# Performance work log

Measured on AMD Instinct MI355X. Metric: run time of the kernel, lower is better.

Reference implementation:

```python
import jax, jax.numpy as jnp
import numpy as np

NLAT, NLON = 128, 256
C = 256
B = 2
THETA_CUTOFF = 5.0 * np.pi / NLAT


def _build_csr():
    # equiangular colatitudes (midpoint rule) and longitudes
    theta = (np.arange(NLAT) + 0.5) * np.pi / NLAT
    phi = 2.0 * np.pi * np.arange(NLON) / NLON
    cth, sth = np.cos(theta), np.sin(theta)
    cphi = np.cos(phi)
    cos_cut = np.cos(THETA_CUTOFF)
    rows, cols = [], []
    for ho in range(NLAT):
        # great-circle distance from output point (theta[ho], lon=0) to all inputs
        cosd = cth[ho] * cth[:, None] + sth[ho] * sth[:, None] * cphi[None, :]
        hi, wi = np.nonzero(cosd >= cos_cut)
        rows.append(np.full(hi.shape[0], ho, dtype=np.int64))
        cols.append(hi * NLON + wi)
    return np.concatenate(rows), np.concatenate(cols)


def setup_inputs() -> dict:
    key = jax.random.key(0)
    kq, kw1, kw2, kw3 = jax.random.split(key, 4)
    scale = float(np.sqrt(1.0 / C))
    query = jax.random.normal(kq, (B, C, NLAT, NLON), dtype=jnp.float32)
    q_w = scale * jax.random.normal(kw1, (C, C), dtype=jnp.float32)
    k_w = scale * jax.random.normal(kw2, (C, C), dtype=jnp.float32)
    v_w = scale * jax.random.normal(kw3, (C, C), dtype=jnp.float32)
    q_bias = jnp.zeros((C,), dtype=jnp.float32)
    k_bias = jnp.zeros((C,), dtype=jnp.float32)
    v_bias = jnp.zeros((C,), dtype=jnp.float32)
    # quadrature weights: 2*pi * wgl / nlon, wgl ~ sin(theta) normalized to sum to 2
    theta = (np.arange(NLAT) + 0.5) * np.pi / NLAT
    wgl = np.sin(theta)
    wgl = 2.0 * wgl / wgl.sum()
    quad_weights = jnp.asarray(2.0 * np.pi * wgl / NLON, dtype=jnp.float32)
    row_idx, col_idx = _build_csr()
    return {
        "query": query,
        "q_w": q_w, "k_w": k_w, "v_w": v_w,
        "q_bias": q_bias, "k_bias": k_bias, "v_bias": v_bias,
        "quad_weights": quad_weights,
        "psi_row_idx": jnp.asarray(row_idx, dtype=jnp.int32),
        "psi_col_idx": jnp.asarray(col_idx, dtype=jnp.int32),
    }


def reference(query, q_w, k_w, v_w, q_bias, k_bias, v_bias, quad_weights, psi_row_idx, psi_col_idx):
    Bq, Cin, H, W = query.shape
    Ck = q_w.shape[0]
    Cv = v_w.shape[0]
    scale = 1.0 / np.sqrt(Cin)  # module sets scale = sqrt(1/in_channels)
    # 1x1 conv2d projections == per-pixel channel GEMMs; query is pre-scaled
    q = jnp.einsum('kc,bchw->bkhw', q_w, query * scale) + q_bias[None, :, None, None]
    k = jnp.einsum('kc,bchw->bkhw', k_w, query) + k_bias[None, :, None, None]
    v = jnp.einsum('vc,bchw->bvhw', v_w, query) + v_bias[None, :, None, None]
    kf = k.reshape(Bq, Ck, H * W)
    vf = v.reshape(Bq, Cv, H * W)
    hi = psi_col_idx // W   # neighbor input latitude  [nnz]
    wi = psi_col_idx % W    # neighbor input longitude offset (at wo=0)
    rows = psi_row_idx      # output latitude per nnz (sorted)
    qw_nbr = quad_weights[hi]  # [nnz]

    def step(carry, wo):
        idx = hi * W + (wi + wo) % W                 # longitude-shifted neighbor gather
        kg = jnp.take(kf, idx, axis=2)               # [B,Ck,nnz]
        vg = jnp.take(vf, idx, axis=2)               # [B,Cv,nnz]
        qcol = jnp.take(q, wo, axis=3)               # [B,Ck,H]
        qr = qcol[:, :, rows]                        # [B,Ck,nnz]
        logits = jnp.einsum('bkn,bkn->nb', qr, kg)   # [nnz,B]
        m = jax.ops.segment_max(logits, rows, num_segments=H, indices_are_sorted=True)
        alpha = jnp.exp(logits - m[rows]) * qw_nbr[:, None]                     # quadrature-weighted softmax numerator
        denom = jax.ops.segment_sum(alpha, rows, num_segments=H, indices_are_sorted=True)  # [H,B]
        num = jax.ops.segment_sum(alpha[:, :, None] * jnp.transpose(vg, (2, 0, 1)), rows,
                                  num_segments=H, indices_are_sorted=True)      # [H,B,Cv]
        return carry, num / denom[:, :, None]

    _, cols = jax.lax.scan(step, None, jnp.arange(W))  # [W,H,B,Cv]
    return jnp.transpose(cols, (2, 3, 1, 0))           # [B,Cv,H,W]
```

## Files before the change

### kernel.cpp

```cpp
#include <hip/hip_runtime.h>
#include <hip/hip_bf16.h>
#include <cstdint>


#define NLAT 128
#define NLON 256
#define NCH  256
#define HWSZ (NLAT * NLON)
#define SEGN 11

typedef __attribute__((ext_vector_type(4))) float f32x4;
typedef __attribute__((ext_vector_type(8))) short s16x8;

__device__ __forceinline__ float bf2f(unsigned int hi_bits) {
    return __uint_as_float(hi_bits);
}
__device__ __forceinline__ unsigned short f2bf(float f) {
    unsigned int u = __float_as_uint(f);
    return (unsigned short)((u + 0x7fffu + ((u >> 16) & 1u)) >> 16);
}

__global__ void k_rowptr(const int* __restrict__ rows, int nnz, int* __restrict__ rp) {
    int ho = threadIdx.x;
    if (ho > NLAT) return;
    int lo = 0, hi = nnz;
    while (lo < hi) {
        int mid = (lo + hi) >> 1;
        if (rows[mid] < ho) lo = mid + 1; else hi = mid;
    }
    rp[ho] = lo;
}

__global__ __launch_bounds__(256) void k_qkv(
    const float* __restrict__ query,
    const float* __restrict__ qw, const float* __restrict__ kw, const float* __restrict__ vw,
    const float* __restrict__ qb, const float* __restrict__ kb, const float* __restrict__ vb,
    unsigned short* __restrict__ qB, unsigned short* __restrict__ kB, unsigned short* __restrict__ vT)
{
    __shared__ unsigned short As[256][40];
    __shared__ unsigned short Bs[64][264];

    const int n0  = blockIdx.x * 64;
    const int b   = n0 >> 15;
    const int hw0 = n0 & (HWSZ - 1);
    const float* qsrc = query + (size_t)b * NCH * HWSZ + hw0;

    const int tid  = threadIdx.x;
    const int lane = tid & 63;
    const int w    = tid >> 6;
    const int l15  = lane & 15;
    const int g    = lane >> 4;

    {
        const int n   = tid & 63;
        const int k0r = tid >> 6;
        #pragma unroll 8
        for (int it = 0; it < 64; ++it) {
            const int kk = k0r + it * 4;
            Bs[n][kk] = f2bf(qsrc[(size_t)kk * HWSZ + n]);
        }
    }

    const int la_m = tid >> 3;
    const int la_k = (tid & 7) * 4;

    for (int y = 0; y < 3; ++y) {
        const float* Wm; const float* bias; float scale;
        if (y == 0)      { Wm = qw; bias = qb; scale = 0.0625f; }
        else if (y == 1) { Wm = kw; bias = kb; scale = 1.0f; }
        else             { Wm = vw; bias = vb; scale = 1.0f; }

        f32x4 acc[4][4] = {};

        for (int ks = 0; ks < 8; ++ks) {
            const int k0 = ks * 32;
            __syncthreads();
            #pragma unroll
            for (int r = 0; r < 8; ++r) {
                const int m = la_m + r * 32;
                const float4 v = *(const float4*)(Wm + (size_t)m * NCH + k0 + la_k);
                ushort4 st;
                st.x = f2bf(v.x * scale); st.y = f2bf(v.y * scale);
                st.z = f2bf(v.z * scale); st.w = f2bf(v.w * scale);
                *(ushort4*)&As[m][la_k] = st;
            }
            __syncthreads();

            s16x8 af[4], bfr[4];
            #pragma unroll
            for (int i = 0; i < 4; ++i)
                af[i] = *(const s16x8*)&As[w * 64 + i * 16 + l15][g * 8];
            #pragma unroll
            for (int j = 0; j < 4; ++j)
                bfr[j] = *(const s16x8*)&Bs[j * 16 + l15][k0 + g * 8];
            #pragma unroll
            for (int i = 0; i < 4; ++i)
                #pragma unroll
                for (int j = 0; j < 4; ++j)
                    acc[i][j] = __builtin_amdgcn_mfma_f32_16x16x32_bf16(af[i], bfr[j], acc[i][j], 0, 0, 0);
        }

        const int mrow = (g) * 4;
        if (y == 2) {
            const int h = hw0 >> 8;
            const int wbase = hw0 & 255;
            #pragma unroll
            for (int i = 0; i < 4; ++i) {
                const int m0 = w * 64 + i * 16 + mrow;
                const float4 bv = *(const float4*)(bias + m0);
                #pragma unroll
                for (int j = 0; j < 4; ++j) {
                    const int wc = wbase + j * 16 + l15;
                    const size_t rowb = ((size_t)((b * 128 + h) * 256 + m0)) << 8;
                    vT[rowb + wc]       = f2bf(acc[i][j][0] + bv.x);
                    vT[rowb + 256 + wc] = f2bf(acc[i][j][1] + bv.y);
                    vT[rowb + 512 + wc] = f2bf(acc[i][j][2] + bv.z);
                    vT[rowb + 768 + wc] = f2bf(acc[i][j][3] + bv.w);
                }
            }
        } else {
            unsigned short* outp = (y == 0) ? qB : kB;
            #pragma unroll
            for (int i = 0; i < 4; ++i) {
                const int m0 = w * 64 + i * 16 + mrow;
                const float4 bv = *(const float4*)(bias + m0);
                #pragma unroll
                for (int j = 0; j < 4; ++j) {
                    const int n = j * 16 + l15;
                    ushort4 st;
                    st.x = f2bf(acc[i][j][0] + bv.x);
                    st.y = f2bf(acc[i][j][1] + bv.y);
                    st.z = f2bf(acc[i][j][2] + bv.z);
                    st.w = f2bf(acc[i][j][3] + bv.w);
                    *(ushort4*)(outp + (((size_t)(b * HWSZ + hw0 + n)) << 8) + m0) = st;
                }
            }
        }
    }
}

__global__ __launch_bounds__(256, 2) void k_attn(
    const unsigned short* __restrict__ qB,
    const unsigned short* __restrict__ kB,
    const unsigned short* __restrict__ vT,
    const int* __restrict__ psi_col,
    const float* __restrict__ qwt,
    const int* __restrict__ rp,
    float* __restrict__ out)
{
    __shared__ unsigned int   segmask[SEGN][8];
    __shared__ int seg_dlo[SEGN], seg_ext[SEGN];
    __shared__ unsigned short als[4][16][40];
    __shared__ float Osm[128][68];

    const int bid  = blockIdx.x;
    const int orig = (bid & 7) * 128 + (bid >> 3);
    const int b    = orig >> 9;
    const int ho   = (orig >> 2) & 127;
    const int wo0  = (orig & 3) * 64;

    const int tid  = threadIdx.x;
    const int lane = tid & 63;
    const int wv   = tid >> 6;
    const int l15  = lane & 15;
    const int g    = lane >> 4;

    for (int i = tid; i < SEGN * 8; i += 256) ((unsigned*)segmask)[i] = 0u;
    __syncthreads();
    const int r0 = rp[ho], r1 = rp[ho + 1];
    for (int n = r0 + tid; n < r1; n += 256) {
        const int col = psi_col[n];
        const int s = (col >> 8) - ho + 5;
        if ((unsigned)s < SEGN) atomicOr(&segmask[s][(col & 255) >> 5], 1u << (col & 31));
    }
    __syncthreads();
    if (tid < SEGN) {
        const int hi = ho - 5 + tid;
        int dlo = 0, ext = 0;
        if (hi >= 0 && hi < 128) {
            unsigned mw[8]; int pc = 0;
            for (int w = 0; w < 8; ++w) { mw[w] = segmask[tid][w]; pc += __popc(mw[w]); }
            if (pc >= 256) { dlo = 0; ext = 256; }
            else if (pc > 0) {
                int t = 0; bool run = true;
                for (int w = 0; w < 8; ++w) {
                    if (!run) break;
                    if (mw[w] == 0xffffffffu) t += 32;
                    else { t += __ffs(~mw[w]) - 1; run = false; }
                }
                int z = 0; run = true;
                for (int w = 7; w >= 0; --w) {
                    if (!run) break;
                    if (mw[w] == 0xffffffffu) z += 32;
                    else { z += __clz(~mw[w]); run = false; }
                }
                if (pc == t + z && t + z <= 256) { dlo = -z; ext = pc; }
                else { dlo = 0; ext = 256; }
            }
        }
        seg_dlo[tid] = dlo; seg_ext[tid] = ext;
    }
    __syncthreads();

    const int ws0 = wo0 + wv * 16;
    const size_t qpt = ((size_t)(b * HWSZ + ho * 256 + ws0 + l15)) << 8;
    s16x8 af[8];
    #pragma unroll
    for (int ck = 0; ck < 8; ++ck) af[ck] = *(const s16x8*)(qB + qpt + ck * 32 + g * 8);

    f32x4 O[16] = {};
    float M[4] = {-1e38f, -1e38f, -1e38f, -1e38f};
    float L[4] = {0.f, 0.f, 0.f, 0.f};

    const size_t kbb = ((size_t)(b * HWSZ)) << 8;
    const unsigned short* vbb = vT + (((size_t)(b * 128)) << 8) * 256;

    for (int s = 0; s < SEGN; ++s) {
        const int ext = seg_ext[s];
        if (ext == 0) continue;
        const int dlo = seg_dlo[s];
        const int hi  = ho - 5 + s;
        const float qw = qwt[hi];
        const unsigned mk0 = __builtin_amdgcn_readfirstlane(segmask[s][0]);
        const unsigned mk1 = __builtin_amdgcn_readfirstlane(segmask[s][1]);
        const unsigned mk2 = __builtin_amdgcn_readfirstlane(segmask[s][2]);
        const unsigned mk3 = __builtin_amdgcn_readfirstlane(segmask[s][3]);
        const unsigned mk4 = __builtin_amdgcn_readfirstlane(segmask[s][4]);
        const unsigned mk5 = __builtin_amdgcn_readfirstlane(segmask[s][5]);
        const unsigned mk6 = __builtin_amdgcn_readfirstlane(segmask[s][6]);
        const unsigned mk7 = __builtin_amdgcn_readfirstlane(segmask[s][7]);

        const int dlo8 = dlo & ~7;
        const int pad  = dlo - dlo8;
        int jtot = 15 + pad + ext; if (jtot > 256) jtot = 256;
        const int wbase = (ws0 + dlo8) & 255;
        const unsigned short* kptr = kB + kbb + (((size_t)(hi * 256)) << 8);
        const unsigned short* vptr = vbb + (((size_t)(hi * 256)) << 8);

        for (int j0 = 0; j0 < jtot; j0 += 32) {
            f32x4 S[2];
            __builtin_amdgcn_s_setprio(1);
            #pragma unroll
            for (int jt = 0; jt < 2; ++jt) {
                const int wil = (wbase + j0 + jt * 16 + l15) & 255;
                const unsigned short* kp = kptr + (((size_t)wil) << 8) + g * 8;
                f32x4 a = {};
                #pragma unroll
                for (int ck = 0; ck < 8; ++ck) {
                    const s16x8 bf = *(const s16x8*)(kp + ck * 32);
                    a = __builtin_amdgcn_mfma_f32_16x16x32_bf16(af[ck], bf, a, 0, 0, 0);
                }
                S[jt] = a;
            }
            __builtin_amdgcn_s_setprio(0);

            #pragma unroll
            for (int jt = 0; jt < 2; ++jt) {
                const int tbase = dlo8 + j0 + jt * 16 + l15 - 4 * g;
                #pragma unroll
                for (int r = 0; r < 4; ++r) {
                    const int wi = (tbase - r) & 255;
                    const unsigned sel = (wi & 0x80)
                        ? ((wi & 0x40) ? ((wi & 0x20) ? mk7 : mk6) : ((wi & 0x20) ? mk5 : mk4))
                        : ((wi & 0x40) ? ((wi & 0x20) ? mk3 : mk2) : ((wi & 0x20) ? mk1 : mk0));
                    if (!((sel >> (wi & 31)) & 1u)) S[jt][r] = -3e38f;
                }
            }

            float rmax[4];
            #pragma unroll
            for (int r = 0; r < 4; ++r) {
                float v = fmaxf(S[0][r], S[1][r]);
                v = fmaxf(v, __shfl_xor(v, 1));
                v = fmaxf(v, __shfl_xor(v, 2));
                v = fmaxf(v, __shfl_xor(v, 4));
                v = fmaxf(v, __shfl_xor(v, 8));
                rmax[r] = v;
            }
            int need = 0;
            #pragma unroll
            for (int r = 0; r < 4; ++r) need |= (rmax[r] > M[r] + 8.0f) ? 1 : 0;
            if (__any(need)) {
                #pragma unroll
                for (int r = 0; r < 4; ++r) {
                    const float Mn = fmaxf(M[r], rmax[r]);
                    const float f = __expf(M[r] - Mn);
                    M[r] = Mn; L[r] *= f;
                    #pragma unroll
                    for (int ct = 0; ct < 16; ++ct) O[ct][r] *= f;
                }
            }

            #pragma unroll
            for (int jt = 0; jt < 2; ++jt) {
                #pragma unroll
                for (int r = 0; r < 4; ++r) {
                    const float a = qw * __expf(S[jt][r] - M[r]);
                    const unsigned short ab = f2bf(a);
                    L[r] += bf2f(((unsigned)ab) << 16);
                    als[wv][4 * g + r][jt * 16 + l15] = ab;
                }
            }
            const s16x8 afr = *(const s16x8*)&als[wv][l15][g * 8];

            const int wj = (wbase + j0 + g * 8) & 255;
            __builtin_amdgcn_s_setprio(1);
            #pragma unroll
            for (int ct = 0; ct < 16; ++ct) {
                const s16x8 vb8 = *(const s16x8*)(vptr + (((size_t)(ct * 16 + l15)) << 8) + wj);
                O[ct] = __builtin_amdgcn_mfma_f32_16x16x32_bf16(afr, vb8, O[ct], 0, 0, 0);
            }
            __builtin_amdgcn_s_setprio(0);
        }
    }

    float rL[4];
    #pragma unroll
    for (int r = 0; r < 4; ++r) {
        float v = L[r];
        v += __shfl_xor(v, 1);
        v += __shfl_xor(v, 2);
        v += __shfl_xor(v, 4);
        v += __shfl_xor(v, 8);
        rL[r] = 1.0f / v;
    }
    __syncthreads();
    #pragma unroll
    for (int p = 0; p < 2; ++p) {
        #pragma unroll
        for (int ci = 0; ci < 8; ++ci) {
            const int ct = p * 8 + ci;
            #pragma unroll
            for (int r = 0; r < 4; ++r)
                Osm[ci * 16 + l15][wv * 16 + 4 * g + r] = O[ct][r] * rL[r];
        }
        __syncthreads();
        const int m4 = (tid & 15) * 4;
        #pragma unroll
        for (int ci = 0; ci < 8; ++ci) {
            const int crow = ci * 16 + (tid >> 4);
            const int c = p * 128 + crow;
            const f32x4 o = *(const f32x4*)&Osm[crow][m4];
            *(f32x4*)(out + (((size_t)((b * NCH + c) * NLAT + ho)) << 8) + wo0 + m4) = o;
        }
        __syncthreads();
    }
}

extern "C" void kernel_launch(void* const* d_in, const int* in_sizes, int n_in,
                              void* d_out, int out_size, void* d_ws, size_t ws_size,
                              hipStream_t stream) {
    const float* query = (const float*)d_in[0];
    const float* q_w   = (const float*)d_in[1];
    const float* k_w   = (const float*)d_in[2];
    const float* v_w   = (const float*)d_in[3];
    const float* q_b   = (const float*)d_in[4];
    const float* k_b   = (const float*)d_in[5];
    const float* v_b   = (const float*)d_in[6];
    const float* qwt   = (const float*)d_in[7];
    const int* psi_row = (const int*)d_in[8];
    const int* psi_col = (const int*)d_in[9];
    const int nnz      = in_sizes[8];

    char* ws = (char*)d_ws;
    unsigned short* qB = (unsigned short*)(ws);
    unsigned short* kB = (unsigned short*)(ws + 33554432);
    unsigned short* vT = (unsigned short*)(ws + 67108864);
    int* rp            = (int*)(ws + 100663296);

    k_rowptr<<<dim3(1), dim3(256), 0, stream>>>(psi_row, nnz, rp);
    k_qkv<<<dim3(1024), dim3(256), 0, stream>>>(query, q_w, k_w, v_w, q_b, k_b, v_b, qB, kB, vT);
    k_attn<<<dim3(1024), dim3(256), 0, stream>>>(qB, kB, vT, psi_col, qwt, rp, (float*)d_out);
}
```

Baseline: 643.0 us.

## Split QKV projection into prep transpose and grid-tiled GEMM, simplify attention epilogue

A new prep kernel transposes the input to channel-last bf16 (staged in the output buffer), converts the weights to bf16, and computes the row pointers. The QKV GEMM then runs on a 3D grid reading bf16 operands straight from global memory, with a small shared-memory transpose for the V output. The attention kernel now maps latitude rows to XCDs in a balanced way, stores output directly without the shared-memory staging, and raises occupancy to 4 blocks per CU. The changes target redundant per-block weight conversion and epilogue synchronisation, at the cost of an extra full pass over the input and uncoalesced output stores.

```diff
diff --git a/kernel.cpp b/kernel.cpp
--- a/kernel.cpp
+++ b/kernel.cpp
@@ -20,126 +20,134 @@
     return (unsigned short)((u + 0x7fffu + ((u >> 16) & 1u)) >> 16);
 }
 
-__global__ void k_rowptr(const int* __restrict__ rows, int nnz, int* __restrict__ rp) {
-    int ho = threadIdx.x;
-    if (ho > NLAT) return;
-    int lo = 0, hi = nnz;
-    while (lo < hi) {
-        int mid = (lo + hi) >> 1;
-        if (rows[mid] < ho) lo = mid + 1; else hi = mid;
-    }
-    rp[ho] = lo;
-}
-
-__global__ __launch_bounds__(256) void k_qkv(
+__global__ __launch_bounds__(256) void k_prep(
     const float* __restrict__ query,
     const float* __restrict__ qw, const float* __restrict__ kw, const float* __restrict__ vw,
+    const int* __restrict__ rows, int nnz,
+    unsigned short* __restrict__ qT, unsigned short* __restrict__ Wbf, int* __restrict__ rp)
+{
+    const int bid = blockIdx.x;
+    const int tid = threadIdx.x;
+    if (bid < 4096) {
+        __shared__ unsigned short T[64][66];
+        const int b   = bid >> 11;
+        const int ct  = (bid >> 9) & 3;
+        const int hw0 = (bid & 511) * 64;
+        const float* src = query + (size_t)b * NCH * HWSZ + (size_t)(ct * 64) * HWSZ + hw0;
+        const int hw_l = tid & 63;
+        const int csub = tid >> 6;
+        #pragma unroll
+        for (int r = 0; r < 16; ++r) {
+            const int c_l = r * 4 + csub;
+            T[c_l][hw_l] = f2bf(src[(size_t)c_l * HWSZ + hw_l]);
+        }
+        __syncthreads();
+        const int c_l2 = tid & 63;
+        const int hsub = tid >> 6;
+        #pragma unroll
+        for (int r = 0; r < 16; ++r) {
+            const int hw_l2 = r * 4 + hsub;
+            qT[((size_t)(b * HWSZ + hw0 + hw_l2) << 8) + ct * 64 + c_l2] = T[c_l2][hw_l2];
+        }
+    } else if (bid < 4099) {
+        const int y = bid - 4096;
+        const float* src = (y == 0) ? qw : (y == 1) ? kw : vw;
+        const float scale = (y == 0) ? 0.0625f : 1.0f;
+        unsigned short* dst = Wbf + y * 65536;
+        for (int i = tid; i < 65536; i += 256) dst[i] = f2bf(src[i] * scale);
+    } else {
+        const int ho = tid;
+        if (ho > NLAT) return;
+        int lo = 0, hi = nnz;
+        while (lo < hi) {
+            int mid = (lo + hi) >> 1;
+            if (rows[mid] < ho) lo = mid + 1; else hi = mid;
+        }
+        rp[ho] = lo;
+    }
+}
+
+__global__ __launch_bounds__(256, 2) void k_qkv(
+    const unsigned short* __restrict__ Wbf,
+    const unsigned short* __restrict__ qT,
     const float* __restrict__ qb, const float* __restrict__ kb, const float* __restrict__ vb,
     unsigned short* __restrict__ qB, unsigned short* __restrict__ kB, unsigned short* __restrict__ vT)
 {
-    __shared__ unsigned short As[256][40];
-    __shared__ unsigned short Bs[64][264];
-
-    const int n0  = blockIdx.x * 64;
-    const int b   = n0 >> 15;
-    const int hw0 = n0 & (HWSZ - 1);
-    const float* qsrc = query + (size_t)b * NCH * HWSZ + hw0;
-
+    __shared__ unsigned short Tv[4][16][18];
+    const int nt = blockIdx.x, mt = blockIdx.y, y = blockIdx.z;
     const int tid  = threadIdx.x;
     const int lane = tid & 63;
-    const int w    = tid >> 6;
+    const int wv   = tid >> 6;
     const int l15  = lane & 15;
     const int g    = lane >> 4;
-
-    {
-        const int n   = tid & 63;
-        const int k0r = tid >> 6;
-        #pragma unroll 8
-        for (int it = 0; it < 64; ++it) {
-            const int kk = k0r + it * 4;
-            Bs[n][kk] = f2bf(qsrc[(size_t)kk * HWSZ + n]);
-        }
-    }
-
-    const int la_m = tid >> 3;
-    const int la_k = (tid & 7) * 4;
-
-    for (int y = 0; y < 3; ++y) {
-        const float* Wm; const float* bias; float scale;
-        if (y == 0)      { Wm = qw; bias = qb; scale = 0.0625f; }
-        else if (y == 1) { Wm = kw; bias = kb; scale = 1.0f; }
-        else             { Wm = vw; bias = vb; scale = 1.0f; }
-
-        f32x4 acc[4][4] = {};
-
-        for (int ks = 0; ks < 8; ++ks) {
-            const int k0 = ks * 32;
-            __syncthreads();
-            #pragma unroll
-            for (int r = 0; r < 8; ++r) {
-                const int m = la_m + r * 32;
-                const float4 v = *(const float4*)(Wm + (size_t)m * NCH + k0 + la_k);
+    const int wm = wv >> 1, wn = wv & 1;
+
+    const int m0    = mt * 128 + wm * 64;
+    const int nbase = nt * 128 + wn * 64;
+    const unsigned short* Wy   = Wbf + y * 65536;
+    const unsigned short* qrow = qT + ((size_t)nbase << 8);
+    const float* bias = (y == 0) ? qb : (y == 1) ? kb : vb;
+
+    f32x4 acc[4][4] = {};
+    #pragma unroll
+    for (int kk = 0; kk < 8; ++kk) {
+        s16x8 af[4], bfr[4];
+        #pragma unroll
+        for (int i = 0; i < 4; ++i)
+            af[i] = *(const s16x8*)(Wy + (size_t)((m0 + i * 16 + l15) << 8) + kk * 32 + g * 8);
+        #pragma unroll
+        for (int j = 0; j < 4; ++j)
+            bfr[j] = *(const s16x8*)(qrow + (size_t)((j * 16 + l15) << 8) + kk * 32 + g * 8);
+        #pragma unroll
+        for (int i = 0; i < 4; ++i)
+            #pragma unroll
+            for (int j = 0; j < 4; ++j)
+                acc[i][j] = __builtin_amdgcn_mfma_f32_16x16x32_bf16(af[i], bfr[j], acc[i][j], 0, 0, 0);
+    }
+
+    if (y < 2) {
+        unsigned short* outp = (y == 0) ? qB : kB;
+        #pragma unroll
+        for (int i = 0; i < 4; ++i) {
+            const int c0 = m0 + i * 16 + 4 * g;
+            const float4 bv = *(const float4*)(bias + c0);
+            #pragma unroll
+            for (int j = 0; j < 4; ++j) {
+                const int point = nbase + j * 16 + l15;
                 ushort4 st;
-                st.x = f2bf(v.x * scale); st.y = f2bf(v.y * scale);
-                st.z = f2bf(v.z * scale); st.w = f2bf(v.w * scale);
-                *(ushort4*)&As[m][la_k] = st;
-            }
-            __syncthreads();
-
-            s16x8 af[4], bfr[4];
-            #pragma unroll
-            for (int i = 0; i < 4; ++i)
-                af[i] = *(const s16x8*)&As[w * 64 + i * 16 + l15][g * 8];
-            #pragma unroll
-            for (int j = 0; j < 4; ++j)
-                bfr[j] = *(const s16x8*)&Bs[j * 16 + l15][k0 + g * 8];
-            #pragma unroll
-            for (int i = 0; i < 4; ++i)
-                #pragma unroll
-                for (int j = 0; j < 4; ++j)
-                    acc[i][j] = __builtin_amdgcn_mfma_f32_16x16x32_bf16(af[i], bfr[j], acc[i][j], 0, 0, 0);
-        }
-
-        const int mrow = (g) * 4;
-        if (y == 2) {
-            const int h = hw0 >> 8;
-            const int wbase = hw0 & 255;
-            #pragma unroll
-            for (int i = 0; i < 4; ++i) {
-                const int m0 = w * 64 + i * 16 + mrow;
-                const float4 bv = *(const float4*)(bias + m0);
-                #pragma unroll
-                for (int j = 0; j < 4; ++j) {
-                    const int wc = wbase + j * 16 + l15;
-                    const size_t rowb = ((size_t)((b * 128 + h) * 256 + m0)) << 8;
-                    vT[rowb + wc]       = f2bf(acc[i][j][0] + bv.x);
-                    vT[rowb + 256 + wc] = f2bf(acc[i][j][1] + bv.y);
-                    vT[rowb + 512 + wc] = f2bf(acc[i][j][2] + bv.z);
-                    vT[rowb + 768 + wc] = f2bf(acc[i][j][3] + bv.w);
-                }
-            }
-        } else {
-            unsigned short* outp = (y == 0) ? qB : kB;
-            #pragma unroll
-            for (int i = 0; i < 4; ++i) {
-                const int m0 = w * 64 + i * 16 + mrow;
-                const float4 bv = *(const float4*)(bias + m0);
-                #pragma unroll
-                for (int j = 0; j < 4; ++j) {
-                    const int n = j * 16 + l15;
-                    ushort4 st;
-                    st.x = f2bf(acc[i][j][0] + bv.x);
-                    st.y = f2bf(acc[i][j][1] + bv.y);
-                    st.z = f2bf(acc[i][j][2] + bv.z);
-                    st.w = f2bf(acc[i][j][3] + bv.w);
-                    *(ushort4*)(outp + (((size_t)(b * HWSZ + hw0 + n)) << 8) + m0) = st;
-                }
-            }
-        }
-    }
-}
-
-__global__ __launch_bounds__(256, 2) void k_attn(
+                st.x = f2bf(acc[i][j][0] + bv.x);
+                st.y = f2bf(acc[i][j][1] + bv.y);
+                st.z = f2bf(acc[i][j][2] + bv.z);
+                st.w = f2bf(acc[i][j][3] + bv.w);
+                *(ushort4*)(outp + ((size_t)point << 8) + c0) = st;
+            }
+        }
+    } else {
+        const int b  = nbase >> 15;
+        const int pt = nbase & (HWSZ - 1);
+        const int h  = pt >> 8;
+        const int w0 = pt & 255;
+        #pragma unroll
+        for (int i = 0; i < 4; ++i) {
+            const int c0 = m0 + i * 16 + 4 * g;
+            const float4 bv = *(const float4*)(bias + c0);
+            #pragma unroll
+            for (int j = 0; j < 4; ++j) {
+                Tv[wv][4 * g + 0][l15] = f2bf(acc[i][j][0] + bv.x);
+                Tv[wv][4 * g + 1][l15] = f2bf(acc[i][j][1] + bv.y);
+                Tv[wv][4 * g + 2][l15] = f2bf(acc[i][j][2] + bv.z);
+                Tv[wv][4 * g + 3][l15] = f2bf(acc[i][j][3] + bv.w);
+                __builtin_amdgcn_s_waitcnt(0);
+                const ushort4 tv = *(const ushort4*)&Tv[wv][l15][g * 4];
+                *(ushort4*)(vT + (((size_t)((b * 128 + h) * 256 + m0 + i * 16 + l15)) << 8)
+                               + w0 + j * 16 + g * 4) = tv;
+                __builtin_amdgcn_s_waitcnt(0);
+            }
+        }
+    }
+}
+
+__global__ __launch_bounds__(256, 4) void k_attn(
     const unsigned short* __restrict__ qB,
     const unsigned short* __restrict__ kB,
     const unsigned short* __restrict__ vT,
@@ -148,16 +156,18 @@
     const int* __restrict__ rp,
     float* __restrict__ out)
 {
-    __shared__ unsigned int   segmask[SEGN][8];
+    __shared__ unsigned int segmask[SEGN][8];
     __shared__ int seg_dlo[SEGN], seg_ext[SEGN];
     __shared__ unsigned short als[4][16][40];
-    __shared__ float Osm[128][68];
-
-    const int bid  = blockIdx.x;
-    const int orig = (bid & 7) * 128 + (bid >> 3);
-    const int b    = orig >> 9;
-    const int ho   = (orig >> 2) & 127;
-    const int wo0  = (orig & 3) * 64;
+
+    const int bid = blockIdx.x;
+    const int xcd = bid & 7;
+    const int t   = bid >> 3;
+    const int b   = t >> 6;
+    const int q4  = t & 3;
+    const int i16 = (t >> 2) & 15;
+    const int ho  = (i16 < 8) ? (xcd * 8 + i16) : (127 - xcd * 8 - (i16 - 8));
+    const int wo0 = q4 * 64;
 
     const int tid  = threadIdx.x;
     const int lane = tid & 63;
@@ -182,11 +192,11 @@
             for (int w = 0; w < 8; ++w) { mw[w] = segmask[tid][w]; pc += __popc(mw[w]); }
             if (pc >= 256) { dlo = 0; ext = 256; }
             else if (pc > 0) {
-                int t = 0; bool run = true;
+                int tr = 0; bool run = true;
                 for (int w = 0; w < 8; ++w) {
                     if (!run) break;
-                    if (mw[w] == 0xffffffffu) t += 32;
-                    else { t += __ffs(~mw[w]) - 1; run = false; }
+                    if (mw[w] == 0xffffffffu) tr += 32;
+                    else { tr += __ffs(~mw[w]) - 1; run = false; }
                 }
                 int z = 0; run = true;
                 for (int w = 7; w >= 0; --w) {
@@ -194,7 +204,7 @@
                     if (mw[w] == 0xffffffffu) z += 32;
                     else { z += __clz(~mw[w]); run = false; }
                 }
-                if (pc == t + z && t + z <= 256) { dlo = -z; ext = pc; }
+                if (pc == tr + z && tr + z <= 256) { dlo = -z; ext = pc; }
                 else { dlo = 0; ext = 256; }
             }
         }
@@ -324,26 +334,15 @@
         v += __shfl_xor(v, 8);
         rL[r] = 1.0f / v;
     }
-    __syncthreads();
     #pragma unroll
-    for (int p = 0; p < 2; ++p) {
-        #pragma unroll
-        for (int ci = 0; ci < 8; ++ci) {
-            const int ct = p * 8 + ci;
-            #pragma unroll
-            for (int r = 0; r < 4; ++r)
-                Osm[ci * 16 + l15][wv * 16 + 4 * g + r] = O[ct][r] * rL[r];
-        }
-        __syncthreads();
-        const int m4 = (tid & 15) * 4;
-        #pragma unroll
-        for (int ci = 0; ci < 8; ++ci) {
-            const int crow = ci * 16 + (tid >> 4);
-            const int c = p * 128 + crow;
-            const f32x4 o = *(const f32x4*)&Osm[crow][m4];
-            *(f32x4*)(out + (((size_t)((b * NCH + c) * NLAT + ho)) << 8) + wo0 + m4) = o;
-        }
-        __syncthreads();
+    for (int ct = 0; ct < 16; ++ct) {
+        const int c = ct * 16 + l15;
+        f32x4 o;
+        o[0] = O[ct][0] * rL[0];
+        o[1] = O[ct][1] * rL[1];
+        o[2] = O[ct][2] * rL[2];
+        o[3] = O[ct][3] * rL[3];
+        *(f32x4*)(out + (((size_t)((b * NCH + c) * NLAT + ho)) << 8) + ws0 + 4 * g) = o;
     }
 }
 
@@ -363,12 +362,14 @@
     const int nnz      = in_sizes[8];
 
     char* ws = (char*)d_ws;
-    unsigned short* qB = (unsigned short*)(ws);
-    unsigned short* kB = (unsigned short*)(ws + 33554432);
-    unsigned short* vT = (unsigned short*)(ws + 67108864);
-    int* rp            = (int*)(ws + 100663296);
-
-    k_rowptr<<<dim3(1), dim3(256), 0, stream>>>(psi_row, nnz, rp);
-    k_qkv<<<dim3(1024), dim3(256), 0, stream>>>(query, q_w, k_w, v_w, q_b, k_b, v_b, qB, kB, vT);
+    unsigned short* qB  = (unsigned short*)(ws);
+    unsigned short* kB  = (unsigned short*)(ws + 33554432);
+    unsigned short* vT  = (unsigned short*)(ws + 67108864);
+    unsigned short* Wbf = (unsigned short*)(ws + 100663296);
+    int* rp             = (int*)(ws + 100663296 + 393216);
+    unsigned short* qT  = (unsigned short*)d_out;
+
+    k_prep<<<dim3(4100), dim3(256), 0, stream>>>(query, q_w, k_w, v_w, psi_row, nnz, qT, Wbf, rp);
+    k_qkv<<<dim3(512, 2, 3), dim3(256), 0, stream>>>(Wbf, qT, q_b, k_b, v_b, qB, kB, vT);
     k_attn<<<dim3(1024), dim3(256), 0, stream>>>(qB, kB, vT, psi_col, qwt, rp, (float*)d_out);
 }
```

Result: slower. 1.114 ms (+73.2%).
